# Optimization experiments

Hardware: AMD Instinct MI355X
Metric: run time of the kernel (lower is better)

## Reference

```python
import jax, jax.numpy as jnp
import numpy as np

HEAD_DIM = 128


def _apply_rotary(x, cos, sin):
    # x: [B, S, H, HD]; cos/sin: [S, HD//2]
    xr = x.reshape(*x.shape[:-1], -1, 2)  # interleaved pairs
    xe, xo = xr[..., 0], xr[..., 1]
    c = cos[None, :, None, :]
    s = sin[None, :, None, :]
    oe = xe * c - xo * s
    oo = xe * s + xo * c
    return jnp.stack([oe, oo], axis=-1).reshape(x.shape)


def setup_inputs() -> dict:
    key = jax.random.key(0)
    ks = jax.random.split(key, 8)
    B, S, D = 2, 1024, 4096
    KVD = 1024  # n_kv_heads * head_dim = 8 * 128
    MAXB, MAXS, KVH, HD = 2, 2048, 8, HEAD_DIM
    theta = 500000.0
    # rotary tables (real/imag of freqs_cis)
    inv = 1.0 / theta ** (np.arange(0, HD, 2)[: HD // 2].astype(np.float32) / HD)
    t = np.arange(S, dtype=np.float32)
    fr = np.outer(t, inv)
    sc = 0.02
    return {
        "x": jax.random.normal(ks[0], (B, S, D), jnp.float32),
        "wq": jax.random.normal(ks[1], (D, D), jnp.float32) * sc,
        "wk": jax.random.normal(ks[2], (D, KVD), jnp.float32) * sc,
        "wv": jax.random.normal(ks[3], (D, KVD), jnp.float32) * sc,
        "wo": jax.random.normal(ks[4], (D, D), jnp.float32) * sc,
        "freqs_cos": jnp.asarray(np.cos(fr)),
        "freqs_sin": jnp.asarray(np.sin(fr)),
        "cache_k": jnp.zeros((MAXB, MAXS, KVH, HD), jnp.float32),
        "cache_v": jnp.zeros((MAXB, MAXS, KVH, HD), jnp.float32),
        "start_pos": 0,
    }


def reference(x, wq, wk, wv, wo, freqs_cos, freqs_sin, cache_k, cache_v, start_pos):
    B, S, D = x.shape
    HD = HEAD_DIM
    H = wq.shape[1] // HD
    KVH = wk.shape[1] // HD
    n_rep = H // KVH

    xq = (x @ wq).reshape(B, S, H, HD)
    xk = (x @ wk).reshape(B, S, KVH, HD)
    xv = (x @ wv).reshape(B, S, KVH, HD)

    xq = _apply_rotary(xq, freqs_cos, freqs_sin)
    xk = _apply_rotary(xk, freqs_cos, freqs_sin)

    # KV-cache update (scatter at start_pos), then read back prefix
    cache_k = cache_k.at[:B, start_pos:start_pos + S].set(xk)
    cache_v = cache_v.at[:B, start_pos:start_pos + S].set(xv)
    keys = cache_k[:B, : start_pos + S]    # [B, T, KVH, HD]
    values = cache_v[:B, : start_pos + S]

    # GQA: repeat kv heads
    keys = jnp.repeat(keys, n_rep, axis=2)      # [B, T, H, HD]
    values = jnp.repeat(values, n_rep, axis=2)

    scale = 1.0 / jnp.sqrt(jnp.float32(HD))
    scores = jnp.einsum("bshd,bthd->bhst", xq, keys) * scale  # [B, H, S, T]

    # causal mask: zeros for the start_pos prefix, upper-triangular -inf after
    T = start_pos + S
    causal = jnp.triu(jnp.full((S, S), -jnp.inf, jnp.float32), k=1)
    mask = jnp.concatenate([jnp.zeros((S, start_pos), jnp.float32), causal], axis=1)  # [S, T]
    scores = scores + mask[None, None, :, :]

    probs = jax.nn.softmax(scores, axis=-1)
    out = jnp.einsum("bhst,bthd->bshd", probs, values).reshape(B, S, D)
    return out @ wo
```

## Files before the change

kernel.cpp:

```cpp
#include <hip/hip_runtime.h>
#include <stdint.h>

#define B_    2
#define S_    1024
#define D_    4096
#define KVD_  1024
#define H_    32
#define KVH_  8
#define HD_   128
#define M_    (B_ * S_)
#define N1_   (D_ + 2 * KVD_)
#define QK_SCALE_L2E (0.08838834764831845f * 1.4426950408889634f)

typedef __attribute__((ext_vector_type(8))) short bf16x8;
typedef __attribute__((ext_vector_type(4))) float f32x4;
typedef __attribute__((ext_vector_type(4))) unsigned short u16x4;
typedef __attribute__((ext_vector_type(8))) unsigned short u16x8;

__device__ inline unsigned short f2bf(float f) {
  unsigned u = __float_as_uint(f);
  u += 0x7FFFu + ((u >> 16) & 1u);
  return (unsigned short)(u >> 16);
}
__device__ inline float bf2f(unsigned short b) {
  return __uint_as_float(((unsigned)b) << 16);
}

#define ASYNC_LD16(g, l) __builtin_amdgcn_global_load_lds( \
    (const __attribute__((address_space(1))) void*)(g),    \
    (__attribute__((address_space(3))) void*)(l), 16, 0, 0)

#define MFMA16(a, b, c) __builtin_amdgcn_mfma_f32_16x16x32_bf16(a, b, c, 0, 0, 0)

#define WAIT_LGKM0() do { asm volatile("s_waitcnt lgkmcnt(0)" ::: "memory"); \
                          __builtin_amdgcn_sched_barrier(0); } while (0)
#define SCHED_PIN() __builtin_amdgcn_sched_barrier(0)
#define BAR() __builtin_amdgcn_s_barrier()

__global__ __launch_bounds__(256) void k_prep(const float* __restrict__ x,
                                              unsigned short* __restrict__ xb,
                                              const float* __restrict__ wq,
                                              const float* __restrict__ wk,
                                              const float* __restrict__ wv,
                                              const float* __restrict__ wo,
                                              unsigned short* __restrict__ w1t,
                                              unsigned short* __restrict__ wot) {
  int bid = blockIdx.x;
  if (bid < 8192) {
    size_t i = ((size_t)bid * 256 + threadIdx.x) * 4;
    float4 v = *(const float4*)(x + i);
    u16x4 o;
    o[0] = f2bf(v.x); o[1] = f2bf(v.y); o[2] = f2bf(v.z); o[3] = f2bf(v.w);
    *(u16x4*)(xb + i) = o;
    return;
  }
  bid -= 8192;
  const float* in; unsigned short* out; int C, bx, by;
  if (bid < 4096)      { in = wq; out = w1t;                          C = 4096; bx = bid & 63; by = bid >> 6; }
  else if (bid < 5120) { bid -= 4096; in = wk; out = w1t + (size_t)D_ * D_;            C = 1024; bx = bid & 15; by = bid >> 4; }
  else if (bid < 6144) { bid -= 5120; in = wv; out = w1t + (size_t)(D_ + KVD_) * D_;   C = 1024; bx = bid & 15; by = bid >> 4; }
  else                 { bid -= 6144; in = wo; out = wot;                              C = 4096; bx = bid & 63; by = bid >> 6; }
  const int R = 4096;
  __shared__ unsigned short tile[64][72];
  int t = threadIdx.x;
  int c0 = bx * 64, r0 = by * 64;
#pragma unroll
  for (int j = 0; j < 4; ++j) {
    int r = (t >> 4) + 16 * j;
    int c = (t & 15) * 4;
    float4 v = *(const float4*)(in + (size_t)(r0 + r) * C + c0 + c);
    tile[r][c + 0] = f2bf(v.x); tile[r][c + 1] = f2bf(v.y);
    tile[r][c + 2] = f2bf(v.z); tile[r][c + 3] = f2bf(v.w);
  }
  __syncthreads();
#pragma unroll
  for (int j = 0; j < 2; ++j) {
    int cc = (t >> 3) + 32 * j;
    int r = (t & 7) * 8;
    u16x8 o;
#pragma unroll
    for (int i = 0; i < 8; ++i) o[i] = tile[r + i][cc];
    *(u16x8*)(out + (size_t)(c0 + cc) * R + r0 + r) = o;
  }
}

__global__ __launch_bounds__(512, 4) void k_gemm_g1(const unsigned short* __restrict__ A,
                                                    const unsigned short* __restrict__ Bt,
                                                    unsigned short* __restrict__ C,
                                                    const float* __restrict__ fc,
                                                    const float* __restrict__ fs) {
  __shared__ unsigned short L[40960];
  const int tid = threadIdx.x, lane = tid & 63, w = tid >> 6;
  const int l15 = lane & 15, l4 = lane >> 4;
  const int wm = w >> 2, wn = w & 3;
  const int brow = blockIdx.y * 128, bcol = blockIdx.x * 192;
  const unsigned short* gA = A + (size_t)brow * 4096;
  const unsigned short* gB = Bt + (size_t)bcol * 4096;
  const int scol = ((lane & 7) ^ (lane >> 3)) * 8;

#define G1_ST_A(bb, kt, r) ASYNC_LD16( \
    gA + (size_t)((r) * 64 + w * 8 + (lane >> 3)) * 4096 + (kt) * 64 + scol, \
    L + (bb) + ((r) * 64 + w * 8) * 64)
#define G1_ST_B(bb, kt, r) ASYNC_LD16( \
    gB + (size_t)((r) * 64 + w * 8 + (lane >> 3)) * 4096 + (kt) * 64 + scol, \
    L + (bb) + 8192 + ((r) * 64 + w * 8) * 64)

  f32x4 acc[4][3] = {};
  bf16x8 bfr[3][2], af[2][2];

  G1_ST_A(0, 0, 0); G1_ST_A(0, 0, 1);
  G1_ST_B(0, 0, 0); G1_ST_B(0, 0, 1); G1_ST_B(0, 0, 2);
  G1_ST_B(20480, 1, 0); G1_ST_B(20480, 1, 1); G1_ST_B(20480, 1, 2);
  asm volatile("s_waitcnt vmcnt(3)" ::: "memory");
  SCHED_PIN();
  BAR();

  for (int t = 0; t < 64; ++t) {
    const int cb = (t & 1) * 20480, nb = cb ^ 20480;

#pragma unroll
    for (int nf = 0; nf < 3; ++nf)
#pragma unroll
      for (int ks = 0; ks < 2; ++ks)
        bfr[nf][ks] = *(const bf16x8*)(L + cb + 8192 +
            (wn * 48 + nf * 16 + l15) * 64 + ((ks * 4 + l4) ^ (l15 & 7)) * 8);
#pragma unroll
    for (int i = 0; i < 2; ++i)
#pragma unroll
      for (int ks = 0; ks < 2; ++ks)
        af[i][ks] = *(const bf16x8*)(L + cb +
            (wm * 64 + i * 16 + l15) * 64 + ((ks * 4 + l4) ^ (l15 & 7)) * 8);
    if (t + 1 < 64) { G1_ST_A(nb, t + 1, 0); G1_ST_A(nb, t + 1, 1); }
    SCHED_PIN(); BAR(); WAIT_LGKM0();
    __builtin_amdgcn_s_setprio(1);
#pragma unroll
    for (int i = 0; i < 2; ++i)
#pragma unroll
      for (int nf = 0; nf < 3; ++nf)
#pragma unroll
        for (int ks = 0; ks < 2; ++ks)
          acc[i][nf] = MFMA16(af[i][ks], bfr[nf][ks], acc[i][nf]);
    __builtin_amdgcn_s_setprio(0);
    BAR();

#pragma unroll
    for (int i = 0; i < 2; ++i)
#pragma unroll
      for (int ks = 0; ks < 2; ++ks)
        af[i][ks] = *(const bf16x8*)(L + cb +
            (wm * 64 + (2 + i) * 16 + l15) * 64 + ((ks * 4 + l4) ^ (l15 & 7)) * 8);
    if (t + 2 < 64) { G1_ST_B(cb, t + 2, 0); G1_ST_B(cb, t + 2, 1); G1_ST_B(cb, t + 2, 2); }
    SCHED_PIN(); BAR(); WAIT_LGKM0();
    __builtin_amdgcn_s_setprio(1);
#pragma unroll
    for (int i = 0; i < 2; ++i)
#pragma unroll
      for (int nf = 0; nf < 3; ++nf)
#pragma unroll
        for (int ks = 0; ks < 2; ++ks)
          acc[2 + i][nf] = MFMA16(af[i][ks], bfr[nf][ks], acc[2 + i][nf]);
    __builtin_amdgcn_s_setprio(0);
    if (t + 2 < 64) { asm volatile("s_waitcnt vmcnt(3)" ::: "memory"); }
    else            { asm volatile("s_waitcnt vmcnt(0)" ::: "memory"); }
    SCHED_PIN();
    BAR();
  }
#undef G1_ST_A
#undef G1_ST_B

#pragma unroll
  for (int mf = 0; mf < 4; ++mf)
#pragma unroll
    for (int nf = 0; nf < 3; ++nf)
#pragma unroll
      for (int q = 0; q < 4; ++q) {
        int row = brow + wm * 64 + mf * 16 + l4 * 4 + q;
        int col = bcol + wn * 48 + nf * 16 + l15;
        float v = acc[mf][nf][q];
        float p = __shfl_xor(v, 1);
        float r;
        if (col < D_ + KVD_) {
          int i = (col & 127) >> 1, s = row & (S_ - 1);
          float c = fc[s * 64 + i], sn = fs[s * 64 + i];
          bool ev = (col & 1) == 0;
          float xe = ev ? v : p, xo = ev ? p : v;
          r = ev ? (xe * c - xo * sn) : (xe * sn + xo * c);
          if (col < D_) r *= QK_SCALE_L2E;
        } else r = v;
        C[(size_t)row * N1_ + col] = f2bf(r);
      }
}

__global__ __launch_bounds__(512, 2) void k_gemm_g2(const unsigned short* __restrict__ A,
                                                    const unsigned short* __restrict__ Bt,
                                                    float* __restrict__ C) {
  __shared__ unsigned short L[2 * 24576];
  const int tid = threadIdx.x, lane = tid & 63, w = tid >> 6;
  const int l15 = lane & 15, l4 = lane >> 4;
  const int wm = w >> 2, wn = w & 3;
  const int brow = blockIdx.y * 128, bcol = blockIdx.x * 256;
  const unsigned short* gA = A + (size_t)brow * 4096;
  const unsigned short* gB = Bt + (size_t)bcol * 4096;
  const int srow = lane >> 3;
  const int scol = ((lane & 7) ^ (srow & 7)) * 8;

#define G2_ST_A(buf, kt, r0) ASYNC_LD16( \
    gA + (size_t)((r0) + w * 8 + srow) * 4096 + (kt) * 64 + scol, \
    L + (buf) * 24576 + ((r0) + w * 8) * 64)
#define G2_ST_B(buf, kt, r0) ASYNC_LD16( \
    gB + (size_t)((r0) + w * 8 + srow) * 4096 + (kt) * 64 + scol, \
    L + (buf) * 24576 + 8192 + ((r0) + w * 8) * 64)
#define G2_ST_TILE(buf, kt) do { \
    G2_ST_A(buf, kt, 0); G2_ST_A(buf, kt, 64); \
    G2_ST_B(buf, kt, 0); G2_ST_B(buf, kt, 64); G2_ST_B(buf, kt, 128); G2_ST_B(buf, kt, 192); } while (0)

  const int aoff0 = (wm * 64 + l15) * 64 + ((l4 + 0) ^ (l15 & 7)) * 8;
  const int aoff1 = (wm * 64 + l15) * 64 + ((l4 + 4) ^ (l15 & 7)) * 8;
  const int boff0 = 8192 + (wn * 64 + l15) * 64 + ((l4 + 0) ^ (l15 & 7)) * 8;
  const int boff1 = 8192 + (wn * 64 + l15) * 64 + ((l4 + 4) ^ (l15 & 7)) * 8;

  f32x4 acc[4][4] = {};

  G2_ST_TILE(0, 0);
  G2_ST_TILE(1, 1);
  asm volatile("s_waitcnt vmcnt(6)" ::: "memory");
  BAR();

  for (int t = 0; t < 64; ++t) {
    const unsigned short* Lc = L + (t & 1) * 24576;
    bf16x8 af[4], bk[4];

#pragma unroll
    for (int m = 0; m < 4; ++m) af[m] = *(const bf16x8*)(Lc + aoff0 + m * 1024);
#pragma unroll
    for (int n = 0; n < 4; ++n) bk[n] = *(const bf16x8*)(Lc + boff0 + n * 1024);
    SCHED_PIN(); BAR(); WAIT_LGKM0();
    __builtin_amdgcn_s_setprio(1);
#pragma unroll
    for (int m = 0; m < 4; ++m)
#pragma unroll
      for (int n = 0; n < 4; ++n) acc[m][n] = MFMA16(af[m], bk[n], acc[m][n]);
    __builtin_amdgcn_s_setprio(0);
    BAR();

#pragma unroll
    for (int m = 0; m < 4; ++m) af[m] = *(const bf16x8*)(Lc + aoff1 + m * 1024);
#pragma unroll
    for (int n = 0; n < 4; ++n) bk[n] = *(const bf16x8*)(Lc + boff1 + n * 1024);
    SCHED_PIN(); BAR(); WAIT_LGKM0();
    __builtin_amdgcn_s_setprio(1);
#pragma unroll
    for (int m = 0; m < 4; ++m)
#pragma unroll
      for (int n = 0; n < 4; ++n) acc[m][n] = MFMA16(af[m], bk[n], acc[m][n]);
    __builtin_amdgcn_s_setprio(0);
    SCHED_PIN();
    if (t + 2 < 64) {
      G2_ST_TILE(t & 1, t + 2);
      asm volatile("s_waitcnt vmcnt(6)" ::: "memory");
    } else if (t + 1 < 64) {
      asm volatile("s_waitcnt vmcnt(0)" ::: "memory");
    }
    BAR();
  }
#undef G2_ST_TILE
#undef G2_ST_A
#undef G2_ST_B

#pragma unroll
  for (int mf = 0; mf < 4; ++mf)
#pragma unroll
    for (int nf = 0; nf < 4; ++nf)
#pragma unroll
      for (int q = 0; q < 4; ++q) {
        int row = brow + wm * 64 + mf * 16 + l4 * 4 + q;
        int col = bcol + wn * 64 + nf * 16 + l15;
        C[(size_t)row * D_ + col] = acc[mf][nf][q];
      }
}

__global__ __launch_bounds__(256) void k_transpose_v(const unsigned short* __restrict__ qkv,
                                                     unsigned short* __restrict__ vt) {
  int bh = blockIdx.z;
  int d0 = blockIdx.x * 64;
  int s0 = blockIdx.y * 64;
  __shared__ unsigned short tile[64][72];
  int t = threadIdx.x;
  const unsigned short* src = qkv + (size_t)(bh >> 3) * S_ * N1_ + D_ + KVD_ + (bh & 7) * HD_;
#pragma unroll
  for (int j = 0; j < 2; ++j) {
    int s = (t >> 3) + 32 * j;
    int d = (t & 7) * 8;
    u16x8 v = *(const u16x8*)(src + (size_t)(s0 + s) * N1_ + d0 + d);
#pragma unroll
    for (int i = 0; i < 8; ++i) tile[s][d + i] = v[i];
  }
  __syncthreads();
#pragma unroll
  for (int j = 0; j < 2; ++j) {
    int d = (t >> 3) + 32 * j;
    int s = (t & 7) * 8;
    u16x8 o;
#pragma unroll
    for (int i = 0; i < 8; ++i) o[i] = tile[s + i][d];
    *(u16x8*)(vt + (size_t)(bh * HD_ + d0 + d) * S_ + s0 + s) = o;
  }
}

__global__ __launch_bounds__(256) void k_flash(const unsigned short* __restrict__ qkv,
                                               const unsigned short* __restrict__ vt,
                                               unsigned short* __restrict__ ao) {
  int f = blockIdx.x;
  int bh = f >> 3;
  int qt = (f & 256) ? (7 - (f & 7)) : (f & 7);
  int b = bh >> 5, h = bh & 31;
  int kh = h >> 2;
  int tid = threadIdx.x, lane = tid & 63, w = tid >> 6;
  int l15 = lane & 15, l4 = lane >> 4;

  __shared__ unsigned short Ks[2 * 64 * 128];
  __shared__ unsigned short Vs[2 * 128 * 64];
  __shared__ unsigned short Ps[4][32 * 64];

  int qb0 = qt * 128;
  int rwb = qb0 + w * 32;
  int NT = 2 * qt + 2;

  const unsigned short* qp = qkv + (size_t)(b * S_ + rwb) * N1_ + h * HD_;
  bf16x8 qf[2][4];
#pragma unroll
  for (int qr = 0; qr < 2; ++qr)
#pragma unroll
    for (int ks = 0; ks < 4; ++ks)
      qf[qr][ks] = *(const bf16x8*)(qp + (size_t)(qr * 16 + l15) * N1_ + ks * 32 + l4 * 8);

  f32x4 o[2][8];
#pragma unroll
  for (int qr = 0; qr < 2; ++qr)
#pragma unroll
    for (int d = 0; d < 8; ++d) o[qr][d] = (f32x4){0.f, 0.f, 0.f, 0.f};
  float lrun[2][4];
#pragma unroll
  for (int qr = 0; qr < 2; ++qr)
#pragma unroll
    for (int q = 0; q < 4; ++q) lrun[qr][q] = 0.f;

  const unsigned short* kbase = qkv + (size_t)(b * S_) * N1_ + D_ + kh * HD_;
  const unsigned short* vbase = vt + (size_t)(b * KVH_ + kh) * HD_ * S_;
  int krl = lane >> 4, kcu = lane & 15;
  int vrl = lane >> 3, vcu = lane & 7;

#define STAGE_KV(bo, itt) do {                                               \
    int kv0s = (itt) * 64;                                                   \
    _Pragma("unroll")                                                        \
    for (int j = 0; j < 4; ++j) {                                            \
      int kc = w * 4 + j;                                                    \
      int krow = kc * 4 + krl;                                               \
      int su = kcu ^ (krow & 7);                                             \
      ASYNC_LD16(kbase + (size_t)(kv0s + krow) * N1_ + su * 8,               \
                 Ks + (bo) * 8192 + kc * 512);                               \
      int vrow = kc * 8 + vrl;                                               \
      int sv = vcu ^ (vrow & 7);                                             \
      ASYNC_LD16(vbase + (size_t)vrow * S_ + kv0s + sv * 8,                  \
                 Vs + (bo) * 8192 + kc * 512);                               \
    }                                                                        \
  } while (0)

  int cur = 0;
  STAGE_KV(0, 0);

  for (int it = 0; it < NT; ++it) {
    int kv0 = it * 64;
    if (it + 1 < NT) {
      STAGE_KV(cur ^ 1, it + 1);
      asm volatile("s_waitcnt vmcnt(8)" ::: "memory");
    } else {
      asm volatile("s_waitcnt vmcnt(0)" ::: "memory");
    }
    __builtin_amdgcn_s_barrier();
    __builtin_amdgcn_sched_barrier(0);

    if (kv0 <= rwb + 31) {
      const unsigned short* Kc = Ks + cur * 8192;
      const unsigned short* Vc = Vs + cur * 8192;

      f32x4 sf[2][4] = {};
      __builtin_amdgcn_s_setprio(1);
#pragma unroll
      for (int ks = 0; ks < 4; ++ks)
#pragma unroll
        for (int n = 0; n < 4; ++n) {
          int row = n * 16 + l15;
          int u = (l4 + ks * 4) ^ (row & 7);
          bf16x8 kf = *(const bf16x8*)(Kc + row * 128 + u * 8);
          sf[0][n] = MFMA16(qf[0][ks], kf, sf[0][n]);
          sf[1][n] = MFMA16(qf[1][ks], kf, sf[1][n]);
        }
      __builtin_amdgcn_s_setprio(0);

      if (kv0 + 63 > rwb) {
#pragma unroll
        for (int qr = 0; qr < 2; ++qr)
#pragma unroll
          for (int n = 0; n < 4; ++n)
#pragma unroll
            for (int q = 0; q < 4; ++q) {
              int rq = rwb + qr * 16 + l4 * 4 + q;
              int ck = kv0 + n * 16 + l15;
              if (ck > rq) sf[qr][n][q] = -1e30f;
            }
      }

#pragma unroll
      for (int qr = 0; qr < 2; ++qr)
#pragma unroll
        for (int n = 0; n < 4; ++n)
#pragma unroll
          for (int q = 0; q < 4; ++q) {
            float p = __builtin_amdgcn_exp2f(sf[qr][n][q]);
            sf[qr][n][q] = p;
            lrun[qr][q] += p;
          }

      unsigned short* pw = Ps[w];
#pragma unroll
      for (int qr = 0; qr < 2; ++qr)
#pragma unroll
        for (int n = 0; n < 4; ++n)
#pragma unroll
          for (int q = 0; q < 4; ++q) {
            int rp = qr * 16 + l4 * 4 + q;
            int cp = n * 16 + l15;
            pw[rp * 64 + (((cp >> 3) ^ (rp & 7)) * 8) + (cp & 7)] = f2bf(sf[qr][n][q]);
          }

      __builtin_amdgcn_s_setprio(1);
#pragma unroll
      for (int kvs = 0; kvs < 2; ++kvs) {
        bf16x8 pa0 = *(const bf16x8*)(pw + (l15) * 64 + (((l4 + kvs * 4) ^ (l15 & 7)) * 8));
        bf16x8 pa1 = *(const bf16x8*)(pw + (16 + l15) * 64 + (((l4 + kvs * 4) ^ (l15 & 7)) * 8));
#pragma unroll
        for (int d = 0; d < 8; ++d) {
          int vrow = d * 16 + l15;
          int u = (l4 + kvs * 4) ^ (vrow & 7);
          bf16x8 vf = *(const bf16x8*)(Vc + vrow * 64 + u * 8);
          o[0][d] = MFMA16(pa0, vf, o[0][d]);
          o[1][d] = MFMA16(pa1, vf, o[1][d]);
        }
      }
      __builtin_amdgcn_s_setprio(0);
    }

    __builtin_amdgcn_s_barrier();
    cur ^= 1;
  }
#undef STAGE_KV

  float invl[2][4];
#pragma unroll
  for (int qr = 0; qr < 2; ++qr)
#pragma unroll
    for (int q = 0; q < 4; ++q) {
      float s = lrun[qr][q];
#pragma unroll
      for (int off = 1; off < 16; off <<= 1) s += __shfl_xor(s, off, 16);
      invl[qr][q] = 1.f / s;
    }
#pragma unroll
  for (int qr = 0; qr < 2; ++qr)
#pragma unroll
    for (int d = 0; d < 8; ++d)
#pragma unroll
      for (int q = 0; q < 4; ++q) {
        int row = b * S_ + rwb + qr * 16 + l4 * 4 + q;
        ao[(size_t)row * D_ + h * HD_ + d * 16 + l15] = f2bf(o[qr][d][q] * invl[qr][q]);
      }
}

extern "C" void kernel_launch(void* const* d_in, const int* in_sizes, int n_in,
                              void* d_out, int out_size, void* d_ws, size_t ws_size,
                              hipStream_t stream) {
  const float* x  = (const float*)d_in[0];
  const float* wq = (const float*)d_in[1];
  const float* wk = (const float*)d_in[2];
  const float* wv = (const float*)d_in[3];
  const float* wo = (const float*)d_in[4];
  const float* fc = (const float*)d_in[5];
  const float* fs = (const float*)d_in[6];
  float* out = (float*)d_out;

  char* ws = (char*)d_ws;
  unsigned short* xb  = (unsigned short*)ws; ws += (size_t)M_ * D_ * 2;
  unsigned short* w1t = (unsigned short*)ws; ws += (size_t)N1_ * D_ * 2;
  unsigned short* wot = (unsigned short*)ws; ws += (size_t)D_ * D_ * 2;
  unsigned short* qkv = (unsigned short*)ws; ws += (size_t)M_ * N1_ * 2;
  unsigned short* vtb = (unsigned short*)ws; ws += (size_t)B_ * KVH_ * HD_ * S_ * 2;
  unsigned short* ao  = (unsigned short*)ws; ws += (size_t)M_ * D_ * 2;

  k_prep<<<18432, 256, 0, stream>>>(x, xb, wq, wk, wv, wo, w1t, wot);

  k_gemm_g1<<<dim3(N1_ / 192, M_ / 128), 512, 0, stream>>>(xb, w1t, qkv, fc, fs);

  k_transpose_v<<<dim3(2, 16, 16), 256, 0, stream>>>(qkv, vtb);
  k_flash<<<dim3(512), 256, 0, stream>>>(qkv, vtb, ao);

  k_gemm_g2<<<dim3(D_ / 256, M_ / 128), 512, 0, stream>>>(ao, wot, out);
}
```

Before: 268.1 us.

## Shrink output GEMM tile to 128x128 with staggered A/B async prefetch

```diff
diff --git a/kernel.cpp b/kernel.cpp
--- a/kernel.cpp
+++ b/kernel.cpp
@@ -191,90 +191,96 @@
       }
 }
 
-__global__ __launch_bounds__(512, 2) void k_gemm_g2(const unsigned short* __restrict__ A,
+__global__ __launch_bounds__(512, 4) void k_gemm_g2(const unsigned short* __restrict__ A,
                                                     const unsigned short* __restrict__ Bt,
                                                     float* __restrict__ C) {
-  __shared__ unsigned short L[2 * 24576];
+  __shared__ unsigned short L[32768];
   const int tid = threadIdx.x, lane = tid & 63, w = tid >> 6;
   const int l15 = lane & 15, l4 = lane >> 4;
   const int wm = w >> 2, wn = w & 3;
-  const int brow = blockIdx.y * 128, bcol = blockIdx.x * 256;
+  const int brow = blockIdx.y * 128, bcol = blockIdx.x * 128;
   const unsigned short* gA = A + (size_t)brow * 4096;
   const unsigned short* gB = Bt + (size_t)bcol * 4096;
-  const int srow = lane >> 3;
-  const int scol = ((lane & 7) ^ (srow & 7)) * 8;
-
-#define G2_ST_A(buf, kt, r0) ASYNC_LD16( \
-    gA + (size_t)((r0) + w * 8 + srow) * 4096 + (kt) * 64 + scol, \
-    L + (buf) * 24576 + ((r0) + w * 8) * 64)
-#define G2_ST_B(buf, kt, r0) ASYNC_LD16( \
-    gB + (size_t)((r0) + w * 8 + srow) * 4096 + (kt) * 64 + scol, \
-    L + (buf) * 24576 + 8192 + ((r0) + w * 8) * 64)
-#define G2_ST_TILE(buf, kt) do { \
-    G2_ST_A(buf, kt, 0); G2_ST_A(buf, kt, 64); \
-    G2_ST_B(buf, kt, 0); G2_ST_B(buf, kt, 64); G2_ST_B(buf, kt, 128); G2_ST_B(buf, kt, 192); } while (0)
-
-  const int aoff0 = (wm * 64 + l15) * 64 + ((l4 + 0) ^ (l15 & 7)) * 8;
-  const int aoff1 = (wm * 64 + l15) * 64 + ((l4 + 4) ^ (l15 & 7)) * 8;
-  const int boff0 = 8192 + (wn * 64 + l15) * 64 + ((l4 + 0) ^ (l15 & 7)) * 8;
-  const int boff1 = 8192 + (wn * 64 + l15) * 64 + ((l4 + 4) ^ (l15 & 7)) * 8;
-
-  f32x4 acc[4][4] = {};
-
-  G2_ST_TILE(0, 0);
-  G2_ST_TILE(1, 1);
-  asm volatile("s_waitcnt vmcnt(6)" ::: "memory");
+  const int scol = ((lane & 7) ^ (lane >> 3)) * 8;
+
+#define G2_ST_A(bb, kt, r) ASYNC_LD16( \
+    gA + (size_t)((r) * 64 + w * 8 + (lane >> 3)) * 4096 + (kt) * 64 + scol, \
+    L + (bb) + ((r) * 64 + w * 8) * 64)
+#define G2_ST_B(bb, kt, r) ASYNC_LD16( \
+    gB + (size_t)((r) * 64 + w * 8 + (lane >> 3)) * 4096 + (kt) * 64 + scol, \
+    L + (bb) + 8192 + ((r) * 64 + w * 8) * 64)
+
+  f32x4 acc[4][2] = {};
+  bf16x8 bfr[2][2], af[2][2];
+
+  G2_ST_A(0, 0, 0); G2_ST_A(0, 0, 1);
+  G2_ST_B(0, 0, 0); G2_ST_B(0, 0, 1);
+  G2_ST_B(16384, 1, 0); G2_ST_B(16384, 1, 1);
+  asm volatile("s_waitcnt vmcnt(2)" ::: "memory");
+  SCHED_PIN();
   BAR();
 
   for (int t = 0; t < 64; ++t) {
-    const unsigned short* Lc = L + (t & 1) * 24576;
-    bf16x8 af[4], bk[4];
-
-#pragma unroll
-    for (int m = 0; m < 4; ++m) af[m] = *(const bf16x8*)(Lc + aoff0 + m * 1024);
-#pragma unroll
-    for (int n = 0; n < 4; ++n) bk[n] = *(const bf16x8*)(Lc + boff0 + n * 1024);
+    const int cb = (t & 1) * 16384, nb = cb ^ 16384;
+
+#pragma unroll
+    for (int nf = 0; nf < 2; ++nf)
+#pragma unroll
+      for (int ks = 0; ks < 2; ++ks)
+        bfr[nf][ks] = *(const bf16x8*)(L + cb + 8192 +
+            (wn * 32 + nf * 16 + l15) * 64 + ((ks * 4 + l4) ^ (l15 & 7)) * 8);
+#pragma unroll
+    for (int i = 0; i < 2; ++i)
+#pragma unroll
+      for (int ks = 0; ks < 2; ++ks)
+        af[i][ks] = *(const bf16x8*)(L + cb +
+            (wm * 64 + i * 16 + l15) * 64 + ((ks * 4 + l4) ^ (l15 & 7)) * 8);
+    if (t + 1 < 64) { G2_ST_A(nb, t + 1, 0); G2_ST_A(nb, t + 1, 1); }
     SCHED_PIN(); BAR(); WAIT_LGKM0();
     __builtin_amdgcn_s_setprio(1);
 #pragma unroll
-    for (int m = 0; m < 4; ++m)
-#pragma unroll
-      for (int n = 0; n < 4; ++n) acc[m][n] = MFMA16(af[m], bk[n], acc[m][n]);
+    for (int i = 0; i < 2; ++i)
+#pragma unroll
+      for (int nf = 0; nf < 2; ++nf)
+#pragma unroll
+        for (int ks = 0; ks < 2; ++ks)
+          acc[i][nf] = MFMA16(af[i][ks], bfr[nf][ks], acc[i][nf]);
     __builtin_amdgcn_s_setprio(0);
     BAR();
 
 #pragma unroll
-    for (int m = 0; m < 4; ++m) af[m] = *(const bf16x8*)(Lc + aoff1 + m * 1024);
-#pragma unroll
-    for (int n = 0; n < 4; ++n) bk[n] = *(const bf16x8*)(Lc + boff1 + n * 1024);
+    for (int i = 0; i < 2; ++i)
+#pragma unroll
+      for (int ks = 0; ks < 2; ++ks)
+        af[i][ks] = *(const bf16x8*)(L + cb +
+            (wm * 64 + (2 + i) * 16 + l15) * 64 + ((ks * 4 + l4) ^ (l15 & 7)) * 8);
+    if (t + 2 < 64) { G2_ST_B(cb, t + 2, 0); G2_ST_B(cb, t + 2, 1); }
     SCHED_PIN(); BAR(); WAIT_LGKM0();
     __builtin_amdgcn_s_setprio(1);
 #pragma unroll
-    for (int m = 0; m < 4; ++m)
-#pragma unroll
-      for (int n = 0; n < 4; ++n) acc[m][n] = MFMA16(af[m], bk[n], acc[m][n]);
+    for (int i = 0; i < 2; ++i)
+#pragma unroll
+      for (int nf = 0; nf < 2; ++nf)
+#pragma unroll
+        for (int ks = 0; ks < 2; ++ks)
+          acc[2 + i][nf] = MFMA16(af[i][ks], bfr[nf][ks], acc[2 + i][nf]);
     __builtin_amdgcn_s_setprio(0);
+    if (t + 2 < 64) { asm volatile("s_waitcnt vmcnt(2)" ::: "memory"); }
+    else            { asm volatile("s_waitcnt vmcnt(0)" ::: "memory"); }
     SCHED_PIN();
-    if (t + 2 < 64) {
-      G2_ST_TILE(t & 1, t + 2);
-      asm volatile("s_waitcnt vmcnt(6)" ::: "memory");
-    } else if (t + 1 < 64) {
-      asm volatile("s_waitcnt vmcnt(0)" ::: "memory");
-    }
     BAR();
   }
-#undef G2_ST_TILE
 #undef G2_ST_A
 #undef G2_ST_B
 
 #pragma unroll
   for (int mf = 0; mf < 4; ++mf)
 #pragma unroll
-    for (int nf = 0; nf < 4; ++nf)
+    for (int nf = 0; nf < 2; ++nf)
 #pragma unroll
       for (int q = 0; q < 4; ++q) {
         int row = brow + wm * 64 + mf * 16 + l4 * 4 + q;
-        int col = bcol + wn * 64 + nf * 16 + l15;
+        int col = bcol + wn * 32 + nf * 16 + l15;
         C[(size_t)row * D_ + col] = acc[mf][nf][q];
       }
 }
@@ -504,5 +510,5 @@
   k_transpose_v<<<dim3(2, 16, 16), 256, 0, stream>>>(qkv, vtb);
   k_flash<<<dim3(512), 256, 0, stream>>>(qkv, vtb, ao);
 
-  k_gemm_g2<<<dim3(D_ / 256, M_ / 128), 512, 0, stream>>>(ao, wot, out);
-}
+  k_gemm_g2<<<dim3(D_ / 128, M_ / 128), 512, 0, stream>>>(ao, wot, out);
+}
```

Result: no change. 263.8 us (median of 2 runs) (-1.6%).
